# Optimization experiments

Measured on AMD Instinct MI355X. Metric: run time of the kernel, lower is better.

Reference implementation:

```python
import jax, jax.numpy as jnp
import numpy as np

H = 128
EPS = 1e-5
INFERENCE_BIAS = 0.1


def setup_inputs() -> dict:
    key = jax.random.key(0)
    ks = jax.random.split(key, 10)
    n_users, n_foods, E = 100000, 50000, 1000000
    z_user = jax.random.normal(ks[0], (n_users, H), dtype=jnp.float32)
    z_food = jax.random.normal(ks[1], (n_foods, H), dtype=jnp.float32)
    row = jax.random.randint(ks[2], (E,), 0, n_users, dtype=jnp.int64)
    col = jax.random.randint(ks[3], (E,), 0, n_foods, dtype=jnp.int64)
    # lin1: Linear(2H -> H); lin2: Linear(H -> 1)
    W1 = jax.random.normal(ks[4], (H, 2 * H), dtype=jnp.float32) * (1.0 / np.sqrt(2 * H))
    b1 = jnp.zeros((H,), dtype=jnp.float32)
    gamma = jnp.ones((H,), dtype=jnp.float32)
    beta = jnp.zeros((H,), dtype=jnp.float32)
    running_mean = jax.random.normal(ks[5], (H,), dtype=jnp.float32) * 0.1
    running_var = jnp.abs(jax.random.normal(ks[6], (H,), dtype=jnp.float32)) * 0.1 + 1.0
    W2 = jax.random.normal(ks[7], (1, H), dtype=jnp.float32) * (1.0 / np.sqrt(H))
    b2 = jnp.zeros((1,), dtype=jnp.float32)
    return {"z_user": z_user, "z_food": z_food, "row": row, "col": col,
            "W1": W1, "b1": b1, "gamma": gamma, "beta": beta,
            "running_mean": running_mean, "running_var": running_var,
            "W2": W2, "b2": b2}


def reference(z_user, z_food, row, col, W1, b1, gamma, beta,
              running_mean, running_var, W2, b2):
    # gather per-edge endpoint embeddings and concat: [E, 2H]
    z = jnp.concatenate([z_user[row], z_food[col]], axis=-1)
    h = z @ W1.T + b1                                        # [E, H]
    # BatchNorm1d in eval mode: running statistics
    h = (h - running_mean) * jax.lax.rsqrt(running_var + EPS) * gamma + beta
    h = jax.nn.relu(h)                                        # dropout is identity in eval
    out = h @ W2.T + b2                                       # [E, 1]
    return jax.nn.sigmoid((out + INFERENCE_BIAS).reshape(-1)) # [E]
```

## Files before the change

### kernel.cpp

```cpp
#include <hip/hip_runtime.h>
#include <hip/hip_bf16.h>
#include <math.h>

#define H 128
#define EPS 1e-5f
#define INF_BIAS 0.1f

typedef __attribute__((ext_vector_type(8))) short bf16x8;
typedef __attribute__((ext_vector_type(4))) float f32x4;

__device__ inline unsigned short f2bf_rne(float f) {
    unsigned u = __float_as_uint(f);
    u += 0x7fffu + ((u >> 16) & 1u);
    return (unsigned short)(u >> 16);
}
__device__ inline float bf2f(unsigned short h) {
    return __uint_as_float(((unsigned)h) << 16);
}
__device__ inline unsigned pack2(float a, float b) {
    return (unsigned)f2bf_rne(a) | ((unsigned)f2bf_rne(b) << 16);
}
__device__ inline float2 unpack2(unsigned v) {
    float2 r;
    r.x = __uint_as_float(v << 16);
    r.y = __uint_as_float(v & 0xffff0000u);
    return r;
}

__global__ void prep_kernel(
    const float* __restrict__ W1, const float* __restrict__ b1,
    const float* __restrict__ gamma, const float* __restrict__ beta,
    const float* __restrict__ rm, const float* __restrict__ rv,
    unsigned short* __restrict__ Wswz_u, unsigned short* __restrict__ Wswz_f,
    float* __restrict__ d_user)
{
    const int f    = blockIdx.x;
    const int half = f >> 4, nt = (f >> 2) & 3, kt = f & 3;
    const int t    = threadIdx.x;
    const int c    = t & 15, q = t >> 4;

    const int j  = half * 64 + (c >> 2) * 16 + nt * 4 + (c & 3);
    const float a = gamma[j] * rsqrtf(rv[j] + EPS);
    const int k0 = kt * 32 + q * 8;

    unsigned short wu[8], wf[8];
    #pragma unroll
    for (int i = 0; i < 8; ++i) {
        wu[i] = f2bf_rne(a * W1[(size_t)j * (2 * H) + k0 + i]);
        wf[i] = f2bf_rne(a * W1[(size_t)j * (2 * H) + H + k0 + i]);
    }
    const size_t dst = (size_t)f * 512 + (size_t)t * 8;
    #pragma unroll
    for (int i = 0; i < 8; ++i) { Wswz_u[dst + i] = wu[i]; Wswz_f[dst + i] = wf[i]; }

    if (kt == 0 && q == 0) d_user[j] = a * (b1[j] - rm[j]) + beta[j];
}

#define TPB 8
__global__ __launch_bounds__(256, 4) void proj_mfma(
    const float* __restrict__ z_user, const float* __restrict__ z_food,
    const unsigned short* __restrict__ Wswz_u, const unsigned short* __restrict__ Wswz_f,
    const float* __restrict__ d_user,
    unsigned short* __restrict__ U, unsigned short* __restrict__ F,
    int n_users, int n_foods, int GU)
{
    const bool userMode = (blockIdx.x < (unsigned)GU);
    const float* Z;
    const unsigned short* Wsrc;
    unsigned short* Out;
    int n, blk0;
    if (userMode) { Z = z_user; Wsrc = Wswz_u; Out = U; n = n_users; blk0 = blockIdx.x; }
    else          { Z = z_food; Wsrc = Wswz_f; Out = F; n = n_foods; blk0 = blockIdx.x - GU; }
    const int tiles = n >> 4;

    const int wave = threadIdx.x >> 6;
    const int lane = threadIdx.x & 63;
    const int c = lane & 15;
    const int q = lane >> 4;
    const int half    = wave & 1;
    const int tilepar = wave >> 1;

    bf16x8 wf[4][4];
    #pragma unroll
    for (int nt = 0; nt < 4; ++nt)
        #pragma unroll
        for (int kt = 0; kt < 4; ++kt)
            wf[nt][kt] = *(const bf16x8*)(Wsrc + (size_t)(half * 16 + nt * 4 + kt) * 512 + lane * 8);

    f32x4 dvec[4];
    #pragma unroll
    for (int nt = 0; nt < 4; ++nt) {
        if (userMode) {
            float4 d = *(const float4*)(d_user + half * 64 + q * 16 + nt * 4);
            dvec[nt] = (f32x4){d.x, d.y, d.z, d.w};
        } else {
            dvec[nt] = (f32x4){0.f, 0.f, 0.f, 0.f};
        }
    }

    #pragma unroll
    for (int it = 0; it < TPB / 2; ++it) {
        const int t = blk0 * TPB + tilepar + it * 2;
        if (t >= tiles) break;

        const int r = t * 16 + c;
        const float* zrow = Z + (size_t)r * H;

        f32x4 acc[4];
        #pragma unroll
        for (int nt = 0; nt < 4; ++nt) acc[nt] = dvec[nt];

        #pragma unroll
        for (int kt = 0; kt < 4; ++kt) {
            const int k0 = kt * 32 + q * 8;
            float4 za = ((const float4*)(zrow + k0))[0];
            float4 zb = ((const float4*)(zrow + k0))[1];
            bf16x8 zhi, zlo;
            {
                float v[8] = {za.x, za.y, za.z, za.w, zb.x, zb.y, zb.z, zb.w};
                #pragma unroll
                for (int i = 0; i < 8; ++i) {
                    unsigned short hi = f2bf_rne(v[i]);
                    unsigned short lo = f2bf_rne(v[i] - bf2f(hi));
                    zhi[i] = (short)hi; zlo[i] = (short)lo;
                }
            }
            #pragma unroll
            for (int nt = 0; nt < 4; ++nt) {
                acc[nt] = __builtin_amdgcn_mfma_f32_16x16x32_bf16(wf[nt][kt], zhi, acc[nt], 0, 0, 0);
                acc[nt] = __builtin_amdgcn_mfma_f32_16x16x32_bf16(wf[nt][kt], zlo, acc[nt], 0, 0, 0);
            }
        }

        unsigned short* obase = Out + (size_t)r * H + half * 64 + q * 16;
        uint4 p0, p1;
        p0.x = pack2(acc[0][0], acc[0][1]); p0.y = pack2(acc[0][2], acc[0][3]);
        p0.z = pack2(acc[1][0], acc[1][1]); p0.w = pack2(acc[1][2], acc[1][3]);
        p1.x = pack2(acc[2][0], acc[2][1]); p1.y = pack2(acc[2][2], acc[2][3]);
        p1.z = pack2(acc[3][0], acc[3][1]); p1.w = pack2(acc[3][2], acc[3][3]);
        *(uint4*)(obase)     = p0;
        *(uint4*)(obase + 8) = p1;
    }
}

#define EUN 4
__global__ __launch_bounds__(256) void edge_kernel(
    const unsigned short* __restrict__ U, const unsigned short* __restrict__ F,
    const int* __restrict__ row, const int* __restrict__ col,
    const float* __restrict__ W2, const float* __restrict__ b2,
    float* __restrict__ out, int E)
{
    const int lane = threadIdx.x & 15;
    const int g  = (blockIdx.x * blockDim.x + threadIdx.x) >> 4;
    const int nG = (gridDim.x * blockDim.x) >> 4;

    const float4 w2a = ((const float4*)W2)[2 * lane];
    const float4 w2b = ((const float4*)W2)[2 * lane + 1];
    const float bias = b2[0] + INF_BIAS;

    for (int e0 = g; e0 < E; e0 += EUN * nG) {
        int iu[EUN], ifo[EUN];
        #pragma unroll
        for (int i = 0; i < EUN; ++i) {
            int e  = e0 + i * nG;
            int ec = (e < E) ? e : e0;
            iu[i]  = row[ec];
            ifo[i] = col[ec];
        }
        uint4 uv[EUN], fv[EUN];
        #pragma unroll
        for (int i = 0; i < EUN; ++i) {
            uv[i] = ((const uint4*)(U + (size_t)iu[i]  * H))[lane];
            fv[i] = ((const uint4*)(F + (size_t)ifo[i] * H))[lane];
        }
        #pragma unroll
        for (int i = 0; i < EUN; ++i) {
            float2 u0 = unpack2(uv[i].x), f0 = unpack2(fv[i].x);
            float2 u1 = unpack2(uv[i].y), f1 = unpack2(fv[i].y);
            float2 u2 = unpack2(uv[i].z), f2 = unpack2(fv[i].z);
            float2 u3 = unpack2(uv[i].w), f3 = unpack2(fv[i].w);

            float s =
                w2a.x * fmaxf(u0.x + f0.x, 0.0f) +
                w2a.y * fmaxf(u0.y + f0.y, 0.0f) +
                w2a.z * fmaxf(u1.x + f1.x, 0.0f) +
                w2a.w * fmaxf(u1.y + f1.y, 0.0f) +
                w2b.x * fmaxf(u2.x + f2.x, 0.0f) +
                w2b.y * fmaxf(u2.y + f2.y, 0.0f) +
                w2b.z * fmaxf(u3.x + f3.x, 0.0f) +
                w2b.w * fmaxf(u3.y + f3.y, 0.0f);

            s += __shfl_xor(s, 8, 16);
            s += __shfl_xor(s, 4, 16);
            s += __shfl_xor(s, 2, 16);
            s += __shfl_xor(s, 1, 16);

            const int e = e0 + i * nG;
            if (lane == 0 && e < E) {
                float x = s + bias;
                out[e] = 1.0f / (1.0f + __expf(-x));
            }
        }
    }
}

extern "C" void kernel_launch(void* const* d_in, const int* in_sizes, int n_in,
                              void* d_out, int out_size, void* d_ws, size_t ws_size,
                              hipStream_t stream) {
    const float* z_user = (const float*)d_in[0];
    const float* z_food = (const float*)d_in[1];
    const int*   row    = (const int*)d_in[2];
    const int*   col    = (const int*)d_in[3];
    const float* W1     = (const float*)d_in[4];
    const float* b1     = (const float*)d_in[5];
    const float* gamma  = (const float*)d_in[6];
    const float* beta   = (const float*)d_in[7];
    const float* rm     = (const float*)d_in[8];
    const float* rv     = (const float*)d_in[9];
    const float* W2     = (const float*)d_in[10];
    const float* b2     = (const float*)d_in[11];
    float* out = (float*)d_out;

    const int n_users = in_sizes[0] / H;
    const int n_foods = in_sizes[1] / H;
    const int E       = in_sizes[2];

    unsigned short* U      = (unsigned short*)d_ws;
    unsigned short* F      = U + (size_t)n_users * H;
    unsigned short* Wswz_u = F + (size_t)n_foods * H;
    unsigned short* Wswz_f = Wswz_u + H * H;
    float*          d_usr  = (float*)(Wswz_f + H * H);

    prep_kernel<<<32, 64, 0, stream>>>(W1, b1, gamma, beta, rm, rv,
                                       Wswz_u, Wswz_f, d_usr);

    const int GU = (n_users + 16 * TPB - 1) / (16 * TPB);
    const int GF = (n_foods + 16 * TPB - 1) / (16 * TPB);
    proj_mfma<<<GU + GF, 256, 0, stream>>>(z_user, z_food, Wswz_u, Wswz_f, d_usr,
                                           U, F, n_users, n_foods, GU);

    edge_kernel<<<8192, 256, 0, stream>>>(U, F, row, col, W2, b2, out, E);
}
```

Baseline: 229.2 us.

## Make projection kernel persistent with double-buffered Z row prefetch

The projection kernel now runs on a fixed grid of 512 blocks (342 for users, 170 for foods) and walks tiles with a grid stride. Each wave keeps two register buffers of Z rows so the next tile's loads are in flight while the current tile goes through the MFMA work. This is meant to hide global load latency and spread the split-weight loads over many tiles. In exchange it needs more registers (launch bounds drop from 4 to 2 blocks per SM) and does redundant clamped loads and compute for tiles past the end.

```diff
diff --git a/kernel.cpp b/kernel.cpp
--- a/kernel.cpp
+++ b/kernel.cpp
@@ -56,29 +56,30 @@
     if (kt == 0 && q == 0) d_user[j] = a * (b1[j] - rm[j]) + beta[j];
 }
 
-#define TPB 8
-__global__ __launch_bounds__(256, 4) void proj_mfma(
+__global__ __launch_bounds__(256, 2) void proj_mfma(
     const float* __restrict__ z_user, const float* __restrict__ z_food,
     const unsigned short* __restrict__ Wswz_u, const unsigned short* __restrict__ Wswz_f,
     const float* __restrict__ d_user,
     unsigned short* __restrict__ U, unsigned short* __restrict__ F,
-    int n_users, int n_foods, int GU)
+    int n_users, int n_foods, int GU, int GB)
 {
     const bool userMode = (blockIdx.x < (unsigned)GU);
     const float* Z;
     const unsigned short* Wsrc;
     unsigned short* Out;
-    int n, blk0;
-    if (userMode) { Z = z_user; Wsrc = Wswz_u; Out = U; n = n_users; blk0 = blockIdx.x; }
-    else          { Z = z_food; Wsrc = Wswz_f; Out = F; n = n_foods; blk0 = blockIdx.x - GU; }
+    int n, blk0, nblk;
+    if (userMode) { Z = z_user; Wsrc = Wswz_u; Out = U; n = n_users; blk0 = blockIdx.x;      nblk = GU; }
+    else          { Z = z_food; Wsrc = Wswz_f; Out = F; n = n_foods; blk0 = blockIdx.x - GU; nblk = GB - GU; }
     const int tiles = n >> 4;
 
     const int wave = threadIdx.x >> 6;
     const int lane = threadIdx.x & 63;
     const int c = lane & 15;
     const int q = lane >> 4;
-    const int half    = wave & 1;
-    const int tilepar = wave >> 1;
+    const int wg   = blk0 * 4 + wave;
+    const int half = wg & 1;
+    const int pair = wg >> 1;
+    const int stride = nblk * 2;
 
     bf16x8 wf[4][4];
     #pragma unroll
@@ -98,26 +99,28 @@
         }
     }
 
-    #pragma unroll
-    for (int it = 0; it < TPB / 2; ++it) {
-        const int t = blk0 * TPB + tilepar + it * 2;
-        if (t >= tiles) break;
-
-        const int r = t * 16 + c;
-        const float* zrow = Z + (size_t)r * H;
-
-        f32x4 acc[4];
-        #pragma unroll
-        for (int nt = 0; nt < 4; ++nt) acc[nt] = dvec[nt];
-
+    auto loadZ = [&](int t, float4 zb[8]) {
+        const float* zrow = Z + (size_t)(min(t, tiles - 1) * 16 + c) * H;
         #pragma unroll
         for (int kt = 0; kt < 4; ++kt) {
             const int k0 = kt * 32 + q * 8;
-            float4 za = ((const float4*)(zrow + k0))[0];
-            float4 zb = ((const float4*)(zrow + k0))[1];
+            zb[2 * kt + 0] = ((const float4*)(zrow + k0))[0];
+            zb[2 * kt + 1] = ((const float4*)(zrow + k0))[1];
+        }
+    };
+
+    auto computeStore = [&](int t, const float4 zb[8]) {
+        f32x4 acc[4];
+        #pragma unroll
+        for (int nt = 0; nt < 4; ++nt) acc[nt] = dvec[nt];
+
+        #pragma unroll
+        for (int kt = 0; kt < 4; ++kt) {
+            float4 za = zb[2 * kt + 0];
+            float4 zv = zb[2 * kt + 1];
             bf16x8 zhi, zlo;
             {
-                float v[8] = {za.x, za.y, za.z, za.w, zb.x, zb.y, zb.z, zb.w};
+                float v[8] = {za.x, za.y, za.z, za.w, zv.x, zv.y, zv.z, zv.w};
                 #pragma unroll
                 for (int i = 0; i < 8; ++i) {
                     unsigned short hi = f2bf_rne(v[i]);
@@ -132,14 +135,31 @@
             }
         }
 
-        unsigned short* obase = Out + (size_t)r * H + half * 64 + q * 16;
-        uint4 p0, p1;
-        p0.x = pack2(acc[0][0], acc[0][1]); p0.y = pack2(acc[0][2], acc[0][3]);
-        p0.z = pack2(acc[1][0], acc[1][1]); p0.w = pack2(acc[1][2], acc[1][3]);
-        p1.x = pack2(acc[2][0], acc[2][1]); p1.y = pack2(acc[2][2], acc[2][3]);
-        p1.z = pack2(acc[3][0], acc[3][1]); p1.w = pack2(acc[3][2], acc[3][3]);
-        *(uint4*)(obase)     = p0;
-        *(uint4*)(obase + 8) = p1;
+        if (t < tiles) {
+            const int r = t * 16 + c;
+            unsigned short* obase = Out + (size_t)r * H + half * 64 + q * 16;
+            uint4 p0, p1;
+            p0.x = pack2(acc[0][0], acc[0][1]); p0.y = pack2(acc[0][2], acc[0][3]);
+            p0.z = pack2(acc[1][0], acc[1][1]); p0.w = pack2(acc[1][2], acc[1][3]);
+            p1.x = pack2(acc[2][0], acc[2][1]); p1.y = pack2(acc[2][2], acc[2][3]);
+            p1.z = pack2(acc[3][0], acc[3][1]); p1.w = pack2(acc[3][2], acc[3][3]);
+            *(uint4*)(obase)     = p0;
+            *(uint4*)(obase + 8) = p1;
+        }
+    };
+
+    int nIt = (tiles + stride - 1) / stride;
+    nIt = (nIt + 1) & ~1;
+
+    float4 zb0[8], zb1[8];
+    int t = pair;
+    loadZ(t, zb0);
+    for (int it = 0; it < nIt; it += 2) {
+        loadZ(t + stride, zb1);
+        computeStore(t, zb0);
+        if (it + 2 < nIt) loadZ(t + 2 * stride, zb0);
+        computeStore(t + stride, zb1);
+        t += 2 * stride;
     }
 }
 
@@ -234,10 +254,9 @@
     prep_kernel<<<32, 64, 0, stream>>>(W1, b1, gamma, beta, rm, rv,
                                        Wswz_u, Wswz_f, d_usr);
 
-    const int GU = (n_users + 16 * TPB - 1) / (16 * TPB);
-    const int GF = (n_foods + 16 * TPB - 1) / (16 * TPB);
-    proj_mfma<<<GU + GF, 256, 0, stream>>>(z_user, z_food, Wswz_u, Wswz_f, d_usr,
-                                           U, F, n_users, n_foods, GU);
+    const int GU = 342, GB = 512;
+    proj_mfma<<<GB, 256, 0, stream>>>(z_user, z_food, Wswz_u, Wswz_f, d_usr,
+                                      U, F, n_users, n_foods, GU, GB);
 
     edge_kernel<<<8192, 256, 0, stream>>>(U, F, row, col, W2, b2, out, E);
 }
```

New measurement: 205.7 us. 1.11x faster.
